# Kernel tuning notes

Hardware: AMD Instinct MI355X
Metric: run time of the kernel (lower is better)

Reference implementation:

```python
import jax, jax.numpy as jnp
import numpy as np

BINS = 30
MMT = 0.75
LOSS_WEIGHT = 1.0
N, C = 2000000, 16


def setup_inputs() -> dict:
    key = jax.random.key(0)
    k1, k2 = jax.random.split(key)
    pred = jax.random.normal(k1, (N, C), dtype=jnp.float32)
    target = jax.random.randint(k2, (N, C), 0, 2, dtype=jnp.int32)
    acc_sum = jnp.zeros((BINS,), dtype=jnp.float32)
    return {"pred": pred, "target": target, "acc_sum": acc_sum}


def reference(pred, target, acc_sum):
    t = target.astype(pred.dtype)
    tot = float(pred.size)

    # gradient density g = |sigmoid(pred) - target|, detached
    g = jnp.abs(jax.nn.sigmoid(jax.lax.stop_gradient(pred)) - t)

    # edges are i/BINS, last edge bumped by 1e-6 => bin = floor(g*BINS), clipped
    idx = jnp.clip((g * BINS).astype(jnp.int32), 0, BINS - 1)  # [N, C]

    flat_idx = idx.reshape(-1)
    counts = jax.ops.segment_sum(
        jnp.ones_like(flat_idx, dtype=pred.dtype), flat_idx, num_segments=BINS
    )  # [BINS]

    nonempty = counts > 0
    new_acc = jnp.where(nonempty, MMT * acc_sum + (1.0 - MMT) * counts, acc_sum)
    safe_acc = jnp.where(nonempty, new_acc, jnp.ones_like(new_acc))

    n = jnp.maximum(jnp.sum(nonempty).astype(pred.dtype), 1.0)
    per_bin_w = tot / safe_acc / n  # [BINS]
    weights = jax.lax.stop_gradient(per_bin_w[idx])  # [N, C]

    # stable BCE with logits: t*softplus(-x) + (1-t)*softplus(x)
    bce = t * jax.nn.softplus(-pred) + (1.0 - t) * jax.nn.softplus(pred)
    loss = jnp.sum(bce * weights) / tot
    return loss * LOSS_WEIGHT
```

## Files before the change

kernel.cpp:

```cpp
#include <hip/hip_runtime.h>

#define BINS 30
#define MMT 0.75f
#define LOSS_WEIGHT 1.0f

#define RSTRIDE 31
#define NTHREADS 256
#define NROWS (NTHREADS / 2)
#define HWORDS (NROWS * RSTRIDE)
#define CNT_ONE (1u << 20)
#define SUM_MASK 0xFFFFFu
#define SSCALE 256.0f
#define INV_SSCALE (1.0f / 256.0f)


__global__ __launch_bounds__(NTHREADS, 8) void ghmc_pass1(
                           const float4* __restrict__ pred4,
                           const int4*   __restrict__ tgt4,
                           float*        __restrict__ gS,
                           unsigned int* __restrict__ gC,
                           int nvec, int total) {
    __shared__ unsigned int sH[HWORDS];
    __shared__ unsigned int sPs[4 * BINS];
    __shared__ unsigned int sPc[4 * BINS];
    const int t = threadIdx.x;

    for (int k = t; k < HWORDS; k += NTHREADS) sH[k] = 0u;
    __syncthreads();

    unsigned int* const row = &sH[(t >> 1) * RSTRIDE];

    const int stride = gridDim.x * blockDim.x;
    int i = blockIdx.x * blockDim.x + t;
    if (i < nvec) {
        float4 p  = pred4[i];
        int4   tv = tgt4[i];
        for (;;) {
            int  ni   = i + stride;
            bool more = (ni < nvec);
            int  li   = more ? ni : i;
            float4 pn  = pred4[li];
            int4   tn  = tgt4[li];
            #pragma unroll
            for (int j = 0; j < 4; ++j) {
                float x  = (&p.x)[j];
                int   tt = (&tv.x)[j];
                float z = tt ? -x : x;
                float a = __expf(-fabsf(z));
                float h = 1.0f + a;
                float r = __builtin_amdgcn_rcpf(h);
                float g = (z >= 0.0f) ? r : 1.0f - r;
                float sp = fmaxf(z, 0.0f) + __logf(h);
                int b = (int)(g * 30.0f);
                b = b > (BINS - 1) ? (BINS - 1) : b;
                b = b < 0 ? 0 : b;
                unsigned int v = (unsigned int)(sp * SSCALE + 0.5f) + CNT_ONE;
                atomicAdd(&row[b], v);
            }
            if (!more) break;
            p = pn; tv = tn; i = ni;
        }
    }

    if (blockIdx.x == 0 && t == 0) {
        const float* predf = (const float*)pred4;
        const int*   tgtf  = (const int*)tgt4;
        for (int e = nvec * 4; e < total; ++e) {
            float x  = predf[e];
            int   tt = tgtf[e];
            float z = tt ? -x : x;
            float a = __expf(-fabsf(z));
            float h = 1.0f + a;
            float r = __builtin_amdgcn_rcpf(h);
            float g = (z >= 0.0f) ? r : 1.0f - r;
            float sp = fmaxf(z, 0.0f) + __logf(h);
            int b = (int)(g * 30.0f);
            b = b > (BINS - 1) ? (BINS - 1) : b;
            b = b < 0 ? 0 : b;
            atomicAdd(&row[b], (unsigned int)(sp * SSCALE + 0.5f) + CNT_ONE);
        }
    }
    __syncthreads();

    {
        const int w = t >> 6;
        const int l = t & 63;
        if (l < BINS) {
            unsigned int cs = 0u, ss = 0u;
            const int r0 = w * (NROWS / 4);
            #pragma unroll 8
            for (int r2 = 0; r2 < NROWS / 4; ++r2) {
                unsigned int v = sH[(r0 + r2) * RSTRIDE + l];
                cs += v >> 20;
                ss += v & SUM_MASK;
            }
            sPs[w * BINS + l] = ss;
            sPc[w * BINS + l] = cs;
        }
    }
    __syncthreads();

    if (t < BINS) {
        unsigned int cs = 0u, ss = 0u;
        #pragma unroll
        for (int w = 0; w < 4; ++w) {
            ss += sPs[w * BINS + t];
            cs += sPc[w * BINS + t];
        }
        if (cs != 0u) {
            atomicAdd(&gS[t], (float)ss * INV_SSCALE);
            atomicAdd(&gC[t], cs);
        }
    }
}

__global__ void ghmc_finalize(const float* __restrict__ gS,
                              const unsigned int* __restrict__ gC,
                              const float* __restrict__ acc_sum,
                              float* __restrict__ out, float tot) {
    if (blockIdx.x == 0 && threadIdx.x == 0) {
        int n = 0;
        for (int b = 0; b < BINS; ++b) n += (gC[b] != 0u);
        float nf = fmaxf((float)n, 1.0f);
        float loss = 0.0f;
        for (int b = 0; b < BINS; ++b) {
            if (gC[b] == 0u) continue;
            float c  = (float)gC[b];
            float na = MMT * acc_sum[b] + (1.0f - MMT) * c;
            float w  = tot / na / nf;
            loss += w * gS[b];
        }
        out[0] = (loss / tot) * LOSS_WEIGHT;
    }
}

extern "C" void kernel_launch(void* const* d_in, const int* in_sizes, int n_in,
                              void* d_out, int out_size, void* d_ws, size_t ws_size,
                              hipStream_t stream) {
    const float* pred    = (const float*)d_in[0];
    const int*   target  = (const int*)d_in[1];
    const float* acc_sum = (const float*)d_in[2];

    const int total = in_sizes[0];
    const int nvec  = total / 4;

    float*        gS = (float*)d_ws;
    unsigned int* gC = (unsigned int*)((char*)d_ws + 256);

    hipMemsetAsync(d_ws, 0, 512, stream);

    const int blocks = 2048;
    ghmc_pass1<<<blocks, NTHREADS, 0, stream>>>(
        (const float4*)pred, (const int4*)target, gS, gC, nvec, total);

    ghmc_finalize<<<1, 64, 0, stream>>>(gS, gC, acc_sum, (float*)d_out, (float)total);
}
```

Baseline: 283.6 us.

## Fuse finalize into pass via last-block counter and process eight elements per thread

The separate finalize kernel is removed. The last block to finish, found through an atomic done-counter, now computes the loss with a wave-level ballot and shuffle reduction. Each thread loads two float4/int4 pairs per iteration, which doubles the work per thread, and the grid is halved to 1024 blocks with launch bounds lowered to 4. This saves one kernel launch and raises memory-level parallelism per thread, at the cost of a threadfence plus an atomic per block and fewer resident waves.

```diff
diff --git a/kernel.cpp b/kernel.cpp
--- a/kernel.cpp
+++ b/kernel.cpp
@@ -14,15 +14,32 @@
 #define INV_SSCALE (1.0f / 256.0f)
 
 
-__global__ __launch_bounds__(NTHREADS, 8) void ghmc_pass1(
+__device__ __forceinline__ void ghm_elem(float x, int tt, unsigned int* __restrict__ row) {
+    float z = tt ? -x : x;
+    float a = __expf(-fabsf(z));
+    float h = 1.0f + a;
+    float r = __builtin_amdgcn_rcpf(h);
+    float g = (z >= 0.0f) ? r : 1.0f - r;
+    float sp = fmaxf(z, 0.0f) + __logf(h);
+    int b = (int)(g * 30.0f);
+    b = b > (BINS - 1) ? (BINS - 1) : b;
+    b = b < 0 ? 0 : b;
+    atomicAdd(&row[b], (unsigned int)(sp * SSCALE + 0.5f) + CNT_ONE);
+}
+
+__global__ __launch_bounds__(NTHREADS, 4) void ghmc_pass1(
                            const float4* __restrict__ pred4,
                            const int4*   __restrict__ tgt4,
                            float*        __restrict__ gS,
                            unsigned int* __restrict__ gC,
-                           int nvec, int total) {
+                           unsigned int* __restrict__ gDone,
+                           const float*  __restrict__ acc_sum,
+                           float*        __restrict__ out,
+                           int ngrp, int total, float tot) {
     __shared__ unsigned int sH[HWORDS];
     __shared__ unsigned int sPs[4 * BINS];
     __shared__ unsigned int sPc[4 * BINS];
+    __shared__ unsigned int sLast;
     const int t = threadIdx.x;
 
     for (int k = t; k < HWORDS; k += NTHREADS) sH[k] = 0u;
@@ -30,55 +47,30 @@
 
     unsigned int* const row = &sH[(t >> 1) * RSTRIDE];
 
-    const int stride = gridDim.x * blockDim.x;
-    int i = blockIdx.x * blockDim.x + t;
-    if (i < nvec) {
-        float4 p  = pred4[i];
-        int4   tv = tgt4[i];
+    const int gs = gridDim.x * blockDim.x;
+    int g = blockIdx.x * blockDim.x + t;
+    if (g < ngrp) {
+        float4 p0 = pred4[2 * g],     p1 = pred4[2 * g + 1];
+        int4   q0 = tgt4[2 * g],      q1 = tgt4[2 * g + 1];
         for (;;) {
-            int  ni   = i + stride;
-            bool more = (ni < nvec);
-            int  li   = more ? ni : i;
-            float4 pn  = pred4[li];
-            int4   tn  = tgt4[li];
+            int  gn   = g + gs;
+            bool more = (gn < ngrp);
+            int  gl   = more ? gn : g;
+            float4 p0n = pred4[2 * gl],  p1n = pred4[2 * gl + 1];
+            int4   q0n = tgt4[2 * gl],   q1n = tgt4[2 * gl + 1];
             #pragma unroll
-            for (int j = 0; j < 4; ++j) {
-                float x  = (&p.x)[j];
-                int   tt = (&tv.x)[j];
-                float z = tt ? -x : x;
-                float a = __expf(-fabsf(z));
-                float h = 1.0f + a;
-                float r = __builtin_amdgcn_rcpf(h);
-                float g = (z >= 0.0f) ? r : 1.0f - r;
-                float sp = fmaxf(z, 0.0f) + __logf(h);
-                int b = (int)(g * 30.0f);
-                b = b > (BINS - 1) ? (BINS - 1) : b;
-                b = b < 0 ? 0 : b;
-                unsigned int v = (unsigned int)(sp * SSCALE + 0.5f) + CNT_ONE;
-                atomicAdd(&row[b], v);
-            }
+            for (int j = 0; j < 4; ++j) ghm_elem((&p0.x)[j], (&q0.x)[j], row);
+            #pragma unroll
+            for (int j = 0; j < 4; ++j) ghm_elem((&p1.x)[j], (&q1.x)[j], row);
             if (!more) break;
-            p = pn; tv = tn; i = ni;
+            p0 = p0n; p1 = p1n; q0 = q0n; q1 = q1n; g = gn;
         }
     }
 
     if (blockIdx.x == 0 && t == 0) {
         const float* predf = (const float*)pred4;
         const int*   tgtf  = (const int*)tgt4;
-        for (int e = nvec * 4; e < total; ++e) {
-            float x  = predf[e];
-            int   tt = tgtf[e];
-            float z = tt ? -x : x;
-            float a = __expf(-fabsf(z));
-            float h = 1.0f + a;
-            float r = __builtin_amdgcn_rcpf(h);
-            float g = (z >= 0.0f) ? r : 1.0f - r;
-            float sp = fmaxf(z, 0.0f) + __logf(h);
-            int b = (int)(g * 30.0f);
-            b = b > (BINS - 1) ? (BINS - 1) : b;
-            b = b < 0 ? 0 : b;
-            atomicAdd(&row[b], (unsigned int)(sp * SSCALE + 0.5f) + CNT_ONE);
-        }
+        for (int e = ngrp * 8; e < total; ++e) ghm_elem(predf[e], tgtf[e], row);
     }
     __syncthreads();
 
@@ -111,26 +103,28 @@
             atomicAdd(&gS[t], (float)ss * INV_SSCALE);
             atomicAdd(&gC[t], cs);
         }
+        __threadfence();
     }
-}
+    __syncthreads();
 
-__global__ void ghmc_finalize(const float* __restrict__ gS,
-                              const unsigned int* __restrict__ gC,
-                              const float* __restrict__ acc_sum,
-                              float* __restrict__ out, float tot) {
-    if (blockIdx.x == 0 && threadIdx.x == 0) {
-        int n = 0;
-        for (int b = 0; b < BINS; ++b) n += (gC[b] != 0u);
-        float nf = fmaxf((float)n, 1.0f);
+    if (t == 0) sLast = (atomicAdd(gDone, 1u) == (unsigned int)(gridDim.x - 1)) ? 1u : 0u;
+    __syncthreads();
+    if (sLast && t < 64) {
+        unsigned int c = 0u; float s = 0.0f;
+        if (t < BINS) {
+            c = atomicAdd(&gC[t], 0u);
+            s = atomicAdd(&gS[t], 0.0f);
+        }
+        unsigned long long m = __ballot(t < BINS && c != 0u);
+        float nf = fmaxf((float)__popcll(m), 1.0f);
+        float term = 0.0f;
+        if (t < BINS && c != 0u) {
+            float na = MMT * acc_sum[t] + (1.0f - MMT) * (float)c;
+            term = (tot / na / nf) * s;
+        }
         float loss = 0.0f;
-        for (int b = 0; b < BINS; ++b) {
-            if (gC[b] == 0u) continue;
-            float c  = (float)gC[b];
-            float na = MMT * acc_sum[b] + (1.0f - MMT) * c;
-            float w  = tot / na / nf;
-            loss += w * gS[b];
-        }
-        out[0] = (loss / tot) * LOSS_WEIGHT;
+        for (int b = 0; b < BINS; ++b) loss += __shfl(term, b);
+        if (t == 0) out[0] = (loss / tot) * LOSS_WEIGHT;
     }
 }
 
@@ -142,16 +136,16 @@
     const float* acc_sum = (const float*)d_in[2];
 
     const int total = in_sizes[0];
-    const int nvec  = total / 4;
+    const int ngrp  = total / 8;
 
-    float*        gS = (float*)d_ws;
-    unsigned int* gC = (unsigned int*)((char*)d_ws + 256);
+    float*        gS    = (float*)d_ws;
+    unsigned int* gC    = (unsigned int*)((char*)d_ws + 256);
+    unsigned int* gDone = (unsigned int*)((char*)d_ws + 512);
 
-    hipMemsetAsync(d_ws, 0, 512, stream);
+    hipMemsetAsync(d_ws, 0, 768, stream);
 
-    const int blocks = 2048;
+    const int blocks = 1024;
     ghmc_pass1<<<blocks, NTHREADS, 0, stream>>>(
-        (const float4*)pred, (const int4*)target, gS, gC, nvec, total);
-
-    ghmc_finalize<<<1, 64, 0, stream>>>(gS, gC, acc_sum, (float*)d_out, (float)total);
+        (const float4*)pred, (const int4*)target, gS, gC, gDone, acc_sum,
+        (float*)d_out, ngrp, total, (float)total);
 }
```

Measured after the change: 311.6 us. 1.1x slower.
